# Performance work log

Measured on AMD Instinct MI355X. Metric: run time of the kernel, lower is better.

The kernel has to match this reference:

```python
import jax, jax.numpy as jnp
import numpy as np

HEADS = 8
DIM_HEAD = 64
SCALE = DIM_HEAD ** -0.5


def setup_inputs() -> dict:
    key = jax.random.key(0)
    ks = jax.random.split(key, 8)
    B, Nq, Nk, D = 4, 1024, 2048, 512
    inner = HEADS * DIM_HEAD  # 512
    x = jax.random.normal(ks[0], (B, Nq, D), dtype=jnp.float32)
    context = jax.random.normal(ks[1], (B, Nk, D), dtype=jnp.float32)
    bias = jax.random.normal(ks[2], (B, Nq, Nk), dtype=jnp.float32)
    s = D ** -0.5
    Wq = jax.random.normal(ks[3], (inner, D), dtype=jnp.float32) * s
    Wk = jax.random.normal(ks[4], (inner, D), dtype=jnp.float32) * s
    Wv = jax.random.normal(ks[5], (inner, D), dtype=jnp.float32) * s
    Wo = jax.random.normal(ks[6], (D, inner), dtype=jnp.float32) * s
    bo = jnp.zeros((D,), dtype=jnp.float32)
    return {"x": x, "context": context, "bias": bias,
            "Wq": Wq, "Wk": Wk, "Wv": Wv, "Wo": Wo, "bo": bo}


def reference(x, context, bias, Wq, Wk, Wv, Wo, bo):
    B, Nq, _ = x.shape
    # torch Linear: y = x @ W.T ; reshape (h d) -> b h n d
    q = (x @ Wq.T).reshape(B, Nq, HEADS, DIM_HEAD).transpose(0, 2, 1, 3)
    k = (context @ Wk.T).reshape(B, -1, HEADS, DIM_HEAD).transpose(0, 2, 1, 3)
    v = (context @ Wv.T).reshape(B, -1, HEADS, DIM_HEAD).transpose(0, 2, 1, 3)
    # explicit-score fallback path (bias supplied)
    scores = jnp.einsum('bhqd,bhkd->bhqk', q, k) * SCALE
    scores = scores + bias[:, None, :, :]  # 3D bias -> (B,1,Nq,Nk)
    attn = jax.nn.softmax(scores, axis=-1)
    out = jnp.einsum('bhqk,bhkd->bhqd', attn, v)
    out = out.transpose(0, 2, 1, 3).reshape(B, Nq, HEADS * DIM_HEAD)
    return out @ Wo.T + bo
```

## Files before the change

kernel.cpp:

```cpp
#include <hip/hip_runtime.h>

#define H 8
#define DH 64
#define NQ 1024
#define NK 2048
#define DIN 512
#define B 4
#define KSPLIT 2
#define KRANGE (NK / KSPLIT)
#define KTILES (KRANGE / 64)
#define BHNQ (B * H * NQ)

typedef __bf16 bf16;
typedef __bf16 bf16x8 __attribute__((ext_vector_type(8)));
typedef __bf16 bf16x4 __attribute__((ext_vector_type(4)));
typedef float floatx4 __attribute__((ext_vector_type(4)));

__device__ inline void gload16(const void* g, void* l) {
  __builtin_amdgcn_global_load_lds(
      (const __attribute__((address_space(1))) void*)g,
      (__attribute__((address_space(3))) void*)l, 16, 0, 0);
}

__global__ void cvt_all(const float* __restrict__ x, const float* __restrict__ ctx,
                        const float* __restrict__ wq, const float* __restrict__ wk,
                        const float* __restrict__ wv, const float* __restrict__ wo,
                        bf16* xb, bf16* cb, bf16* wqb, bf16* wkb, bf16* wvb, bf16* wob) {
  long i = ((long)blockIdx.x * 256 + threadIdx.x) * 4;
  const float* s; bf16* d; long o;
  if (i < 2097152)      { s = x;   d = xb;  o = i; }
  else if (i < 6291456) { s = ctx; d = cb;  o = i - 2097152; }
  else if (i < 6553600) { s = wq;  d = wqb; o = i - 6291456; }
  else if (i < 6815744) { s = wk;  d = wkb; o = i - 6553600; }
  else if (i < 7077888) { s = wv;  d = wvb; o = i - 6815744; }
  else                  { s = wo;  d = wob; o = i - 7077888; }
  float4 f = *(const float4*)(s + o);
  bf16x4 v = { (bf16)f.x, (bf16)f.y, (bf16)f.z, (bf16)f.w };
  *(bf16x4*)(d + o) = v;
}

__global__ __launch_bounds__(256) void gemm_qkv(
    const bf16* __restrict__ xb, const bf16* __restrict__ cb,
    const bf16* __restrict__ wqb, const bf16* __restrict__ wkb, const bf16* __restrict__ wvb,
    bf16* __restrict__ qb, bf16* __restrict__ kb, bf16* __restrict__ vtb) {
  const int which = blockIdx.z;
  if (which == 0 && blockIdx.y >= 32) return;
  const bf16* A = (which == 0) ? xb : cb;
  const bf16* W = (which == 0) ? wqb : ((which == 1) ? wkb : wvb);
  bf16* outb = (which == 0) ? qb : ((which == 1) ? kb : vtb);
  const int logT = (which == 0) ? 10 : 11;
  const float scale = (which == 0) ? 0.125f : 1.0f;
  const bool vmode = (which == 2);

  __shared__ bf16 Al[2][128 * 32];
  __shared__ bf16 Bl[2][128 * 32];
  const int t = threadIdx.x;
  const int lane = t & 63, w = t >> 6;
  const int ln = lane & 15, quad = lane >> 4;
  const int wm = (w >> 1) * 64, wn = (w & 1) * 64;
  const int rowBase = blockIdx.y * 128;
  const int colBase = blockIdx.x * 128;

  floatx4 acc[4][4] = {};
  const int c0 = t, c1 = t + 256;
  const int r0 = c0 >> 2, o0 = (c0 & 3) * 8;
  const int r1 = c1 >> 2, o1 = (c1 & 3) * 8;
  const bf16* Ab = A + (size_t)rowBase * DIN;
  const bf16* Wb = W + (size_t)colBase * DIN;

  gload16(Ab + (size_t)r0 * DIN + o0, &Al[0][c0 * 8]);
  gload16(Ab + (size_t)r1 * DIN + o1, &Al[0][c1 * 8]);
  gload16(Wb + (size_t)r0 * DIN + o0, &Bl[0][c0 * 8]);
  gload16(Wb + (size_t)r1 * DIN + o1, &Bl[0][c1 * 8]);
  __syncthreads();

  for (int k0 = 0; k0 < DIN; k0 += 32) {
    const int cur = (k0 >> 5) & 1, nxt = cur ^ 1;
    if (k0 + 32 < DIN) {
      gload16(Ab + (size_t)r0 * DIN + k0 + 32 + o0, &Al[nxt][c0 * 8]);
      gload16(Ab + (size_t)r1 * DIN + k0 + 32 + o1, &Al[nxt][c1 * 8]);
      gload16(Wb + (size_t)r0 * DIN + k0 + 32 + o0, &Bl[nxt][c0 * 8]);
      gload16(Wb + (size_t)r1 * DIN + k0 + 32 + o1, &Bl[nxt][c1 * 8]);
    }
    bf16x8 af[4], bfr[4];
#pragma unroll
    for (int i = 0; i < 4; i++)
      af[i] = *(const bf16x8*)&Al[cur][(wm + i * 16 + ln) * 32 + quad * 8];
#pragma unroll
    for (int j = 0; j < 4; j++)
      bfr[j] = *(const bf16x8*)&Bl[cur][(wn + j * 16 + ln) * 32 + quad * 8];
#pragma unroll
    for (int i = 0; i < 4; i++)
#pragma unroll
      for (int j = 0; j < 4; j++)
        acc[i][j] = __builtin_amdgcn_mfma_f32_16x16x32_bf16(af[i], bfr[j], acc[i][j], 0, 0, 0);
    __syncthreads();
  }

  const int T = 1 << logT;
#pragma unroll
  for (int i = 0; i < 4; i++)
#pragma unroll
    for (int j = 0; j < 4; j++)
#pragma unroll
      for (int r = 0; r < 4; r++) {
        const int m = rowBase + wm + i * 16 + quad * 4 + r;
        const int n = colBase + wn + j * 16 + ln;
        const float v = acc[i][j][r] * scale;
        const int bb = m >> logT, tok = m & (T - 1);
        const int hh = n >> 6, d = n & 63;
        if (!vmode)
          outb[((((size_t)(bb * H + hh)) << logT) + tok) * DH + d] = (bf16)v;
        else
          outb[(((size_t)(bb * H + hh) * DH + d) << logT) + tok] = (bf16)v;
      }
}

__global__ __launch_bounds__(128) void attn_fwd(
    const bf16* __restrict__ q, const bf16* __restrict__ k,
    const bf16* __restrict__ vt, const float* __restrict__ bias,
    float* __restrict__ op0, float* __restrict__ op1, float* __restrict__ lpart) {
  __shared__ bf16 KL[64 * 64];
  __shared__ bf16 VL[64 * 64];
  __shared__ bf16 Pl[2][16 * 64];
  const int tid = threadIdx.x;
  const int lane = tid & 63, w = tid >> 6;
  const int ln = lane & 15, quad = lane >> 4;
  const int hh = blockIdx.y;
  const int b = blockIdx.z >> 1, ks = blockIdx.z & 1;
  const int q0 = blockIdx.x * 32;
  const int k0 = ks * KRANGE;
  const size_t bh = (size_t)b * H + hh;
  const bf16* qp = q + bh * NQ * DH;
  const bf16* kp = k + bh * NK * DH;
  const bf16* vp = vt + bh * DH * NK;
  const float* bp = bias + ((size_t)b * NQ + q0 + w * 16 + quad * 4) * NK + ln;
  bf16* pl = &Pl[w][0];

  bf16x8 qf[2];
#pragma unroll
  for (int kc = 0; kc < 2; kc++)
    qf[kc] = *(const bf16x8*)(qp + (size_t)(q0 + w * 16 + ln) * DH + kc * 32 + quad * 8);

  floatx4 o[4] = {};
  floatx4 lac = {};
  const bf16x8 ones = {(bf16)1.f, (bf16)1.f, (bf16)1.f, (bf16)1.f,
                       (bf16)1.f, (bf16)1.f, (bf16)1.f, (bf16)1.f};
  constexpr float L2E = 1.44269504f;
  constexpr float OFF = 34.6246810f;

  for (int tt = 0; tt < KTILES; tt++) {
    const int nk0 = k0 + tt * 64;
#pragma unroll
    for (int s = 0; s < 4; s++) {
      const int i = s * 128 + tid;
      const int sr = i >> 3, sc = (i & 7) ^ (sr & 7);
      gload16(kp + (size_t)(nk0 + sr) * DH + sc * 8, &KL[i * 8]);
      gload16(vp + (size_t)sr * NK + nk0 + sc * 8, &VL[i * 8]);
    }
    float bc[4][4];
#pragma unroll
    for (int j = 0; j < 4; j++)
#pragma unroll
      for (int r = 0; r < 4; r++)
        bc[j][r] = bp[(size_t)r * NK + nk0 + j * 16];
    __syncthreads();

    floatx4 s4[4];
#pragma unroll
    for (int j = 0; j < 4; j++) {
      s4[j][0] = bc[j][0]; s4[j][1] = bc[j][1];
      s4[j][2] = bc[j][2]; s4[j][3] = bc[j][3];
    }
#pragma unroll
    for (int j = 0; j < 4; j++)
#pragma unroll
      for (int kc = 0; kc < 2; kc++) {
        const int kr = j * 16 + ln;
        bf16x8 kf = *(const bf16x8*)&KL[kr * 64 + (((kc * 4 + quad) ^ (kr & 7)) * 8)];
        s4[j] = __builtin_amdgcn_mfma_f32_16x16x32_bf16(qf[kc], kf, s4[j], 0, 0, 0);
      }

#pragma unroll
    for (int j = 0; j < 4; j++)
#pragma unroll
      for (int r = 0; r < 4; r++)
        s4[j][r] = exp2f(fmaf(s4[j][r], L2E, -OFF));

#pragma unroll
    for (int j = 0; j < 4; j++)
#pragma unroll
      for (int r = 0; r < 4; r++) {
        const int m = quad * 4 + r;
        pl[m * 64 + (((j * 2 + (ln >> 3)) ^ (m & 7)) * 8) + (ln & 7)] = (bf16)s4[j][r];
      }
    asm volatile("s_waitcnt lgkmcnt(0)" ::: "memory");
    bf16x8 pf[2];
#pragma unroll
    for (int kc = 0; kc < 2; kc++)
      pf[kc] = *(const bf16x8*)&pl[ln * 64 + (((kc * 4 + quad) ^ (ln & 7)) * 8)];

#pragma unroll
    for (int kc = 0; kc < 2; kc++)
      lac = __builtin_amdgcn_mfma_f32_16x16x32_bf16(pf[kc], ones, lac, 0, 0, 0);

#pragma unroll
    for (int jn = 0; jn < 4; jn++)
#pragma unroll
      for (int kc = 0; kc < 2; kc++) {
        const int vr = jn * 16 + ln;
        bf16x8 vf = *(const bf16x8*)&VL[vr * 64 + (((kc * 4 + quad) ^ (vr & 7)) * 8)];
        o[jn] = __builtin_amdgcn_mfma_f32_16x16x32_bf16(pf[kc], vf, o[jn], 0, 0, 0);
      }
    __syncthreads();
  }

  float* op = (ks ? op1 : op0) +
              ((size_t)b * NQ + q0 + w * 16 + quad * 4) * DIN + hh * 64 + ln;
#pragma unroll
  for (int jn = 0; jn < 4; jn++)
#pragma unroll
    for (int r = 0; r < 4; r++)
      op[(size_t)r * DIN + jn * 16] = o[jn][r];

  if (ln == 0) {
    float4 lv = {lac[0], lac[1], lac[2], lac[3]};
    *(float4*)&lpart[((size_t)ks * B * H + b * H + hh) * NQ + q0 + w * 16 + quad * 4] = lv;
  }
}

__global__ __launch_bounds__(256) void gemm_out(
    const float* __restrict__ op0, const float* __restrict__ op1,
    const float* __restrict__ lp, const bf16* __restrict__ W,
    float* __restrict__ outf, const float* __restrict__ bo) {
  __shared__ bf16 Al[2][128 * 32];
  __shared__ bf16 Bl[2][128 * 32];
  const int t = threadIdx.x;
  const int lane = t & 63, w = t >> 6;
  const int ln = lane & 15, quad = lane >> 4;
  const int wm = (w >> 1) * 64, wn = (w & 1) * 64;
  const int rowBase = blockIdx.y * 128;
  const int colBase = blockIdx.x * 128;

  floatx4 acc[4][4] = {};
  const int c0 = t, c1 = t + 256;
  const int r0 = c0 >> 2, o0 = (c0 & 3) * 8;
  const int r1 = c1 >> 2, o1 = (c1 & 3) * 8;
  const int m0 = rowBase + r0, m1 = rowBase + r1;
  const bf16* Wb = W + (size_t)colBase * DIN;

  float linv0[8], linv1[8];
#pragma unroll
  for (int h = 0; h < 8; h++) {
    const int i0 = ((m0 >> 10) * H + h) * NQ + (m0 & 1023);
    const int i1 = ((m1 >> 10) * H + h) * NQ + (m1 & 1023);
    linv0[h] = 1.0f / (lp[i0] + lp[BHNQ + i0]);
    linv1[h] = 1.0f / (lp[i1] + lp[BHNQ + i1]);
  }

#define STAGE_A(K0V, BUF)                                                      \
  {                                                                            \
    const float sA = linv0[(K0V) >> 6], sB = linv1[(K0V) >> 6];                \
    const float* pa0 = op0 + (size_t)m0 * DIN + (K0V) + o0;                    \
    const float* pa1 = op1 + (size_t)m0 * DIN + (K0V) + o0;                    \
    const float* pb0 = op0 + (size_t)m1 * DIN + (K0V) + o1;                    \
    const float* pb1 = op1 + (size_t)m1 * DIN + (K0V) + o1;                    \
    float4 xa = *(const float4*)pa0, xb2 = *(const float4*)(pa0 + 4);          \
    float4 ya = *(const float4*)pa1, yb = *(const float4*)(pa1 + 4);           \
    float4 za = *(const float4*)pb0, zb = *(const float4*)(pb0 + 4);           \
    float4 ua = *(const float4*)pb1, ub = *(const float4*)(pb1 + 4);           \
    bf16x8 v0 = {(bf16)((xa.x + ya.x) * sA), (bf16)((xa.y + ya.y) * sA),       \
                 (bf16)((xa.z + ya.z) * sA), (bf16)((xa.w + ya.w) * sA),       \
                 (bf16)((xb2.x + yb.x) * sA), (bf16)((xb2.y + yb.y) * sA),     \
                 (bf16)((xb2.z + yb.z) * sA), (bf16)((xb2.w + yb.w) * sA)};    \
    bf16x8 v1 = {(bf16)((za.x + ua.x) * sB), (bf16)((za.y + ua.y) * sB),       \
                 (bf16)((za.z + ua.z) * sB), (bf16)((za.w + ua.w) * sB),       \
                 (bf16)((zb.x + ub.x) * sB), (bf16)((zb.y + ub.y) * sB),       \
                 (bf16)((zb.z + ub.z) * sB), (bf16)((zb.w + ub.w) * sB)};      \
    *(bf16x8*)&Al[BUF][c0 * 8] = v0;                                           \
    *(bf16x8*)&Al[BUF][c1 * 8] = v1;                                           \
  }

  STAGE_A(0, 0);
  gload16(Wb + (size_t)r0 * DIN + o0, &Bl[0][c0 * 8]);
  gload16(Wb + (size_t)r1 * DIN + o1, &Bl[0][c1 * 8]);
  __syncthreads();

#pragma unroll
  for (int kk = 0; kk < 16; kk++) {
    const int cur = kk & 1, nxt = cur ^ 1;
    if (kk < 15) {
      const int k1 = (kk + 1) * 32;
      STAGE_A(k1, nxt);
      gload16(Wb + (size_t)r0 * DIN + k1 + o0, &Bl[nxt][c0 * 8]);
      gload16(Wb + (size_t)r1 * DIN + k1 + o1, &Bl[nxt][c1 * 8]);
    }
    bf16x8 af[4], bfr[4];
#pragma unroll
    for (int i = 0; i < 4; i++)
      af[i] = *(const bf16x8*)&Al[cur][(wm + i * 16 + ln) * 32 + quad * 8];
#pragma unroll
    for (int j = 0; j < 4; j++)
      bfr[j] = *(const bf16x8*)&Bl[cur][(wn + j * 16 + ln) * 32 + quad * 8];
#pragma unroll
    for (int i = 0; i < 4; i++)
#pragma unroll
      for (int j = 0; j < 4; j++)
        acc[i][j] = __builtin_amdgcn_mfma_f32_16x16x32_bf16(af[i], bfr[j], acc[i][j], 0, 0, 0);
    __syncthreads();
  }
#undef STAGE_A

#pragma unroll
  for (int i = 0; i < 4; i++)
#pragma unroll
    for (int j = 0; j < 4; j++)
#pragma unroll
      for (int r = 0; r < 4; r++) {
        const int m = rowBase + wm + i * 16 + quad * 4 + r;
        const int n = colBase + wn + j * 16 + ln;
        outf[(size_t)m * DIN + n] = acc[i][j][r] + bo[n];
      }
}

extern "C" void kernel_launch(void* const* d_in, const int* in_sizes, int n_in,
                              void* d_out, int out_size, void* d_ws, size_t ws_size,
                              hipStream_t stream) {
  const float* x    = (const float*)d_in[0];
  const float* ctx  = (const float*)d_in[1];
  const float* bias = (const float*)d_in[2];
  const float* Wq   = (const float*)d_in[3];
  const float* Wk   = (const float*)d_in[4];
  const float* Wv   = (const float*)d_in[5];
  const float* Wo   = (const float*)d_in[6];
  const float* bo   = (const float*)d_in[7];
  float* out = (float*)d_out;

  char* p = (char*)d_ws;
  bf16* xb   = (bf16*)(p + 0);
  bf16* cb   = (bf16*)(p + 4194304);
  bf16* wqb  = (bf16*)(p + 12582912);
  bf16* wkb  = (bf16*)(p + 13107200);
  bf16* wvb  = (bf16*)(p + 13631488);
  bf16* wob  = (bf16*)(p + 14155776);
  bf16* qb   = (bf16*)(p + 14680064);
  bf16* kb   = (bf16*)(p + 18874368);
  bf16* vtb  = (bf16*)(p + 27262976);
  float* op1 = (float*)(p + 35651584);
  float* lpart = (float*)(p + 44040192);
  float* op0 = (float*)cb;

  cvt_all<<<7168, 256, 0, stream>>>(x, ctx, Wq, Wk, Wv, Wo, xb, cb, wqb, wkb, wvb, wob);
  gemm_qkv<<<dim3(4, 64, 3), 256, 0, stream>>>(xb, cb, wqb, wkb, wvb, qb, kb, vtb);
  attn_fwd<<<dim3(NQ / 32, H, B * KSPLIT), 128, 0, stream>>>(qb, kb, vtb, bias, op0, op1, lpart);
  gemm_out<<<dim3(4, 32), 256, 0, stream>>>(op0, op1, lpart, wob, out, bo);
}
```

Measured before the change: 211.2 us.

## Retile GEMMs to 64-row blocks and double query rows per attention warp

The QKV and output projection GEMMs switch to 64x128 tiles, doubling the grid so more blocks fill the GPU. The V projection swaps MFMA operands so each lane writes consecutive tokens into the transposed V buffer, aiming for better store coalescing. The attention kernel has each warp handle 32 query rows instead of 16, reusing each K/V LDS fragment across two MFMAs, which halves K/V tile reloads and block count. The cost is more registers per attention thread, which may lower occupancy, and smaller GEMM tiles give less reuse per block.

Result: faster. 196.6 us (-6.9%).

```diff
diff --git a/kernel.cpp b/kernel.cpp
--- a/kernel.cpp
+++ b/kernel.cpp
@@ -44,7 +44,7 @@
     const bf16* __restrict__ wqb, const bf16* __restrict__ wkb, const bf16* __restrict__ wvb,
     bf16* __restrict__ qb, bf16* __restrict__ kb, bf16* __restrict__ vtb) {
   const int which = blockIdx.z;
-  if (which == 0 && blockIdx.y >= 32) return;
+  if (which == 0 && blockIdx.y >= 64) return;
   const bf16* A = (which == 0) ? xb : cb;
   const bf16* W = (which == 0) ? wqb : ((which == 1) ? wkb : wvb);
   bf16* outb = (which == 0) ? qb : ((which == 1) ? kb : vtb);
@@ -52,67 +52,79 @@
   const float scale = (which == 0) ? 0.125f : 1.0f;
   const bool vmode = (which == 2);
 
-  __shared__ bf16 Al[2][128 * 32];
+  __shared__ bf16 Al[2][64 * 32];
   __shared__ bf16 Bl[2][128 * 32];
   const int t = threadIdx.x;
   const int lane = t & 63, w = t >> 6;
   const int ln = lane & 15, quad = lane >> 4;
-  const int wm = (w >> 1) * 64, wn = (w & 1) * 64;
-  const int rowBase = blockIdx.y * 128;
+  const int wm = (w >> 1) * 32, wn = (w & 1) * 64;
+  const int rowBase = blockIdx.y * 64;
   const int colBase = blockIdx.x * 128;
 
-  floatx4 acc[4][4] = {};
+  floatx4 acc[2][4] = {};
+  const int rA = t >> 2, oA = (t & 3) * 8;
   const int c0 = t, c1 = t + 256;
-  const int r0 = c0 >> 2, o0 = (c0 & 3) * 8;
-  const int r1 = c1 >> 2, o1 = (c1 & 3) * 8;
+  const int rB0 = c0 >> 2, oB0 = (c0 & 3) * 8;
+  const int rB1 = c1 >> 2, oB1 = (c1 & 3) * 8;
   const bf16* Ab = A + (size_t)rowBase * DIN;
   const bf16* Wb = W + (size_t)colBase * DIN;
 
-  gload16(Ab + (size_t)r0 * DIN + o0, &Al[0][c0 * 8]);
-  gload16(Ab + (size_t)r1 * DIN + o1, &Al[0][c1 * 8]);
-  gload16(Wb + (size_t)r0 * DIN + o0, &Bl[0][c0 * 8]);
-  gload16(Wb + (size_t)r1 * DIN + o1, &Bl[0][c1 * 8]);
+  gload16(Ab + (size_t)rA * DIN + oA, &Al[0][t * 8]);
+  gload16(Wb + (size_t)rB0 * DIN + oB0, &Bl[0][c0 * 8]);
+  gload16(Wb + (size_t)rB1 * DIN + oB1, &Bl[0][c1 * 8]);
   __syncthreads();
 
   for (int k0 = 0; k0 < DIN; k0 += 32) {
     const int cur = (k0 >> 5) & 1, nxt = cur ^ 1;
     if (k0 + 32 < DIN) {
-      gload16(Ab + (size_t)r0 * DIN + k0 + 32 + o0, &Al[nxt][c0 * 8]);
-      gload16(Ab + (size_t)r1 * DIN + k0 + 32 + o1, &Al[nxt][c1 * 8]);
-      gload16(Wb + (size_t)r0 * DIN + k0 + 32 + o0, &Bl[nxt][c0 * 8]);
-      gload16(Wb + (size_t)r1 * DIN + k0 + 32 + o1, &Bl[nxt][c1 * 8]);
-    }
-    bf16x8 af[4], bfr[4];
-#pragma unroll
-    for (int i = 0; i < 4; i++)
+      gload16(Ab + (size_t)rA * DIN + k0 + 32 + oA, &Al[nxt][t * 8]);
+      gload16(Wb + (size_t)rB0 * DIN + k0 + 32 + oB0, &Bl[nxt][c0 * 8]);
+      gload16(Wb + (size_t)rB1 * DIN + k0 + 32 + oB1, &Bl[nxt][c1 * 8]);
+    }
+    bf16x8 af[2], bfr[4];
+#pragma unroll
+    for (int i = 0; i < 2; i++)
       af[i] = *(const bf16x8*)&Al[cur][(wm + i * 16 + ln) * 32 + quad * 8];
 #pragma unroll
     for (int j = 0; j < 4; j++)
       bfr[j] = *(const bf16x8*)&Bl[cur][(wn + j * 16 + ln) * 32 + quad * 8];
-#pragma unroll
-    for (int i = 0; i < 4; i++)
-#pragma unroll
-      for (int j = 0; j < 4; j++)
-        acc[i][j] = __builtin_amdgcn_mfma_f32_16x16x32_bf16(af[i], bfr[j], acc[i][j], 0, 0, 0);
+    if (!vmode) {
+#pragma unroll
+      for (int i = 0; i < 2; i++)
+#pragma unroll
+        for (int j = 0; j < 4; j++)
+          acc[i][j] = __builtin_amdgcn_mfma_f32_16x16x32_bf16(af[i], bfr[j], acc[i][j], 0, 0, 0);
+    } else {
+#pragma unroll
+      for (int i = 0; i < 2; i++)
+#pragma unroll
+        for (int j = 0; j < 4; j++)
+          acc[i][j] = __builtin_amdgcn_mfma_f32_16x16x32_bf16(bfr[j], af[i], acc[i][j], 0, 0, 0);
+    }
     __syncthreads();
   }
 
   const int T = 1 << logT;
 #pragma unroll
-  for (int i = 0; i < 4; i++)
+  for (int i = 0; i < 2; i++)
 #pragma unroll
     for (int j = 0; j < 4; j++)
 #pragma unroll
       for (int r = 0; r < 4; r++) {
-        const int m = rowBase + wm + i * 16 + quad * 4 + r;
-        const int n = colBase + wn + j * 16 + ln;
-        const float v = acc[i][j][r] * scale;
-        const int bb = m >> logT, tok = m & (T - 1);
-        const int hh = n >> 6, d = n & 63;
-        if (!vmode)
+        if (!vmode) {
+          const int m = rowBase + wm + i * 16 + quad * 4 + r;
+          const int n = colBase + wn + j * 16 + ln;
+          const float v = acc[i][j][r] * scale;
+          const int bb = m >> logT, tok = m & (T - 1);
+          const int hh = n >> 6, d = n & 63;
           outb[((((size_t)(bb * H + hh)) << logT) + tok) * DH + d] = (bf16)v;
-        else
-          outb[(((size_t)(bb * H + hh) * DH + d) << logT) + tok] = (bf16)v;
+        } else {
+          const int dg = colBase + wn + j * 16 + quad * 4 + r;
+          const int m = rowBase + wm + i * 16 + ln;
+          const int bb = m >> logT, tok = m & (T - 1);
+          const int hh = dg >> 6, d = dg & 63;
+          outb[(((size_t)(bb * H + hh) * DH + d) << logT) + tok] = (bf16)acc[i][j][r];
+        }
       }
 }
 
@@ -122,28 +134,29 @@
     float* __restrict__ op0, float* __restrict__ op1, float* __restrict__ lpart) {
   __shared__ bf16 KL[64 * 64];
   __shared__ bf16 VL[64 * 64];
-  __shared__ bf16 Pl[2][16 * 64];
+  __shared__ bf16 Pl[2][2][16 * 64];
   const int tid = threadIdx.x;
   const int lane = tid & 63, w = tid >> 6;
   const int ln = lane & 15, quad = lane >> 4;
   const int hh = blockIdx.y;
   const int b = blockIdx.z >> 1, ks = blockIdx.z & 1;
-  const int q0 = blockIdx.x * 32;
+  const int q0 = blockIdx.x * 64;
   const int k0 = ks * KRANGE;
   const size_t bh = (size_t)b * H + hh;
   const bf16* qp = q + bh * NQ * DH;
   const bf16* kp = k + bh * NK * DH;
   const bf16* vp = vt + bh * DH * NK;
-  const float* bp = bias + ((size_t)b * NQ + q0 + w * 16 + quad * 4) * NK + ln;
-  bf16* pl = &Pl[w][0];
-
-  bf16x8 qf[2];
-#pragma unroll
-  for (int kc = 0; kc < 2; kc++)
-    qf[kc] = *(const bf16x8*)(qp + (size_t)(q0 + w * 16 + ln) * DH + kc * 32 + quad * 8);
-
-  floatx4 o[4] = {};
-  floatx4 lac = {};
+  const float* bp = bias + ((size_t)b * NQ + q0 + w * 32 + quad * 4) * NK + ln;
+
+  bf16x8 qf[2][2];
+#pragma unroll
+  for (int s = 0; s < 2; s++)
+#pragma unroll
+    for (int kc = 0; kc < 2; kc++)
+      qf[s][kc] = *(const bf16x8*)(qp + (size_t)(q0 + w * 32 + s * 16 + ln) * DH + kc * 32 + quad * 8);
+
+  floatx4 o[2][4] = {};
+  floatx4 lac[2] = {};
   const bf16x8 ones = {(bf16)1.f, (bf16)1.f, (bf16)1.f, (bf16)1.f,
                        (bf16)1.f, (bf16)1.f, (bf16)1.f, (bf16)1.f};
   constexpr float L2E = 1.44269504f;
@@ -158,51 +171,64 @@
       gload16(kp + (size_t)(nk0 + sr) * DH + sc * 8, &KL[i * 8]);
       gload16(vp + (size_t)sr * NK + nk0 + sc * 8, &VL[i * 8]);
     }
-    float bc[4][4];
-#pragma unroll
-    for (int j = 0; j < 4; j++)
-#pragma unroll
-      for (int r = 0; r < 4; r++)
-        bc[j][r] = bp[(size_t)r * NK + nk0 + j * 16];
+    float bc[2][4][4];
+#pragma unroll
+    for (int s = 0; s < 2; s++)
+#pragma unroll
+      for (int j = 0; j < 4; j++)
+#pragma unroll
+        for (int r = 0; r < 4; r++)
+          bc[s][j][r] = bp[(size_t)(s * 16 + r) * NK + nk0 + j * 16];
     __syncthreads();
 
-    floatx4 s4[4];
-#pragma unroll
-    for (int j = 0; j < 4; j++) {
-      s4[j][0] = bc[j][0]; s4[j][1] = bc[j][1];
-      s4[j][2] = bc[j][2]; s4[j][3] = bc[j][3];
-    }
+    floatx4 s4[2][4];
+#pragma unroll
+    for (int s = 0; s < 2; s++)
+#pragma unroll
+      for (int j = 0; j < 4; j++) {
+        s4[s][j][0] = bc[s][j][0]; s4[s][j][1] = bc[s][j][1];
+        s4[s][j][2] = bc[s][j][2]; s4[s][j][3] = bc[s][j][3];
+      }
 #pragma unroll
     for (int j = 0; j < 4; j++)
 #pragma unroll
       for (int kc = 0; kc < 2; kc++) {
         const int kr = j * 16 + ln;
         bf16x8 kf = *(const bf16x8*)&KL[kr * 64 + (((kc * 4 + quad) ^ (kr & 7)) * 8)];
-        s4[j] = __builtin_amdgcn_mfma_f32_16x16x32_bf16(qf[kc], kf, s4[j], 0, 0, 0);
-      }
-
-#pragma unroll
-    for (int j = 0; j < 4; j++)
-#pragma unroll
-      for (int r = 0; r < 4; r++)
-        s4[j][r] = exp2f(fmaf(s4[j][r], L2E, -OFF));
-
-#pragma unroll
-    for (int j = 0; j < 4; j++)
-#pragma unroll
-      for (int r = 0; r < 4; r++) {
-        const int m = quad * 4 + r;
-        pl[m * 64 + (((j * 2 + (ln >> 3)) ^ (m & 7)) * 8) + (ln & 7)] = (bf16)s4[j][r];
-      }
+        s4[0][j] = __builtin_amdgcn_mfma_f32_16x16x32_bf16(qf[0][kc], kf, s4[0][j], 0, 0, 0);
+        s4[1][j] = __builtin_amdgcn_mfma_f32_16x16x32_bf16(qf[1][kc], kf, s4[1][j], 0, 0, 0);
+      }
+
+#pragma unroll
+    for (int s = 0; s < 2; s++)
+#pragma unroll
+      for (int j = 0; j < 4; j++)
+#pragma unroll
+        for (int r = 0; r < 4; r++)
+          s4[s][j][r] = exp2f(fmaf(s4[s][j][r], L2E, -OFF));
+
+#pragma unroll
+    for (int s = 0; s < 2; s++)
+#pragma unroll
+      for (int j = 0; j < 4; j++)
+#pragma unroll
+        for (int r = 0; r < 4; r++) {
+          const int m = quad * 4 + r;
+          Pl[w][s][m * 64 + (((j * 2 + (ln >> 3)) ^ (m & 7)) * 8) + (ln & 7)] = (bf16)s4[s][j][r];
+        }
     asm volatile("s_waitcnt lgkmcnt(0)" ::: "memory");
-    bf16x8 pf[2];
-#pragma unroll
-    for (int kc = 0; kc < 2; kc++)
-      pf[kc] = *(const bf16x8*)&pl[ln * 64 + (((kc * 4 + quad) ^ (ln & 7)) * 8)];
-
-#pragma unroll
-    for (int kc = 0; kc < 2; kc++)
-      lac = __builtin_amdgcn_mfma_f32_16x16x32_bf16(pf[kc], ones, lac, 0, 0, 0);
+    bf16x8 pf[2][2];
+#pragma unroll
+    for (int s = 0; s < 2; s++)
+#pragma unroll
+      for (int kc = 0; kc < 2; kc++)
+        pf[s][kc] = *(const bf16x8*)&Pl[w][s][ln * 64 + (((kc * 4 + quad) ^ (ln & 7)) * 8)];
+
+#pragma unroll
+    for (int s = 0; s < 2; s++)
+#pragma unroll
+      for (int kc = 0; kc < 2; kc++)
+        lac[s] = __builtin_amdgcn_mfma_f32_16x16x32_bf16(pf[s][kc], ones, lac[s], 0, 0, 0);
 
 #pragma unroll
     for (int jn = 0; jn < 4; jn++)
@@ -210,22 +236,25 @@
       for (int kc = 0; kc < 2; kc++) {
         const int vr = jn * 16 + ln;
         bf16x8 vf = *(const bf16x8*)&VL[vr * 64 + (((kc * 4 + quad) ^ (vr & 7)) * 8)];
-        o[jn] = __builtin_amdgcn_mfma_f32_16x16x32_bf16(pf[kc], vf, o[jn], 0, 0, 0);
+        o[0][jn] = __builtin_amdgcn_mfma_f32_16x16x32_bf16(pf[0][kc], vf, o[0][jn], 0, 0, 0);
+        o[1][jn] = __builtin_amdgcn_mfma_f32_16x16x32_bf16(pf[1][kc], vf, o[1][jn], 0, 0, 0);
       }
     __syncthreads();
   }
 
-  float* op = (ks ? op1 : op0) +
-              ((size_t)b * NQ + q0 + w * 16 + quad * 4) * DIN + hh * 64 + ln;
-#pragma unroll
-  for (int jn = 0; jn < 4; jn++)
-#pragma unroll
-    for (int r = 0; r < 4; r++)
-      op[(size_t)r * DIN + jn * 16] = o[jn][r];
-
-  if (ln == 0) {
-    float4 lv = {lac[0], lac[1], lac[2], lac[3]};
-    *(float4*)&lpart[((size_t)ks * B * H + b * H + hh) * NQ + q0 + w * 16 + quad * 4] = lv;
+#pragma unroll
+  for (int s = 0; s < 2; s++) {
+    float* op = (ks ? op1 : op0) +
+                ((size_t)b * NQ + q0 + w * 32 + s * 16 + quad * 4) * DIN + hh * 64 + ln;
+#pragma unroll
+    for (int jn = 0; jn < 4; jn++)
+#pragma unroll
+      for (int r = 0; r < 4; r++)
+        op[(size_t)r * DIN + jn * 16] = o[s][jn][r];
+    if (ln == 0) {
+      float4 lv = {lac[s][0], lac[s][1], lac[s][2], lac[s][3]};
+      *(float4*)&lpart[((size_t)ks * B * H + b * H + hh) * NQ + q0 + w * 32 + s * 16 + quad * 4] = lv;
+    }
   }
 }
 
@@ -233,57 +262,47 @@
     const float* __restrict__ op0, const float* __restrict__ op1,
     const float* __restrict__ lp, const bf16* __restrict__ W,
     float* __restrict__ outf, const float* __restrict__ bo) {
-  __shared__ bf16 Al[2][128 * 32];
+  __shared__ bf16 Al[2][64 * 32];
   __shared__ bf16 Bl[2][128 * 32];
   const int t = threadIdx.x;
   const int lane = t & 63, w = t >> 6;
   const int ln = lane & 15, quad = lane >> 4;
-  const int wm = (w >> 1) * 64, wn = (w & 1) * 64;
-  const int rowBase = blockIdx.y * 128;
+  const int wm = (w >> 1) * 32, wn = (w & 1) * 64;
+  const int rowBase = blockIdx.y * 64;
   const int colBase = blockIdx.x * 128;
 
-  floatx4 acc[4][4] = {};
+  floatx4 acc[2][4] = {};
+  const int rA = t >> 2, oA = (t & 3) * 8;
   const int c0 = t, c1 = t + 256;
-  const int r0 = c0 >> 2, o0 = (c0 & 3) * 8;
-  const int r1 = c1 >> 2, o1 = (c1 & 3) * 8;
-  const int m0 = rowBase + r0, m1 = rowBase + r1;
+  const int rB0 = c0 >> 2, oB0 = (c0 & 3) * 8;
+  const int rB1 = c1 >> 2, oB1 = (c1 & 3) * 8;
+  const int m0 = rowBase + rA;
   const bf16* Wb = W + (size_t)colBase * DIN;
 
-  float linv0[8], linv1[8];
+  float linv0[8];
 #pragma unroll
   for (int h = 0; h < 8; h++) {
     const int i0 = ((m0 >> 10) * H + h) * NQ + (m0 & 1023);
-    const int i1 = ((m1 >> 10) * H + h) * NQ + (m1 & 1023);
     linv0[h] = 1.0f / (lp[i0] + lp[BHNQ + i0]);
-    linv1[h] = 1.0f / (lp[i1] + lp[BHNQ + i1]);
   }
 
 #define STAGE_A(K0V, BUF)                                                      \
   {                                                                            \
-    const float sA = linv0[(K0V) >> 6], sB = linv1[(K0V) >> 6];                \
-    const float* pa0 = op0 + (size_t)m0 * DIN + (K0V) + o0;                    \
-    const float* pa1 = op1 + (size_t)m0 * DIN + (K0V) + o0;                    \
-    const float* pb0 = op0 + (size_t)m1 * DIN + (K0V) + o1;                    \
-    const float* pb1 = op1 + (size_t)m1 * DIN + (K0V) + o1;                    \
+    const float sA = linv0[(K0V) >> 6];                                        \
+    const float* pa0 = op0 + (size_t)m0 * DIN + (K0V) + oA;                    \
+    const float* pa1 = op1 + (size_t)m0 * DIN + (K0V) + oA;                    \
     float4 xa = *(const float4*)pa0, xb2 = *(const float4*)(pa0 + 4);          \
     float4 ya = *(const float4*)pa1, yb = *(const float4*)(pa1 + 4);           \
-    float4 za = *(const float4*)pb0, zb = *(const float4*)(pb0 + 4);           \
-    float4 ua = *(const float4*)pb1, ub = *(const float4*)(pb1 + 4);           \
     bf16x8 v0 = {(bf16)((xa.x + ya.x) * sA), (bf16)((xa.y + ya.y) * sA),       \
                  (bf16)((xa.z + ya.z) * sA), (bf16)((xa.w + ya.w) * sA),       \
                  (bf16)((xb2.x + yb.x) * sA), (bf16)((xb2.y + yb.y) * sA),     \
                  (bf16)((xb2.z + yb.z) * sA), (bf16)((xb2.w + yb.w) * sA)};    \
-    bf16x8 v1 = {(bf16)((za.x + ua.x) * sB), (bf16)((za.y + ua.y) * sB),       \
-                 (bf16)((za.z + ua.z) * sB), (bf16)((za.w + ua.w) * sB),       \
-                 (bf16)((zb.x + ub.x) * sB), (bf16)((zb.y + ub.y) * sB),       \
-                 (bf16)((zb.z + ub.z) * sB), (bf16)((zb.w + ub.w) * sB)};      \
-    *(bf16x8*)&Al[BUF][c0 * 8] = v0;                                           \
-    *(bf16x8*)&Al[BUF][c1 * 8] = v1;                                           \
+    *(bf16x8*)&Al[BUF][t * 8] = v0;                                            \
   }
 
   STAGE_A(0, 0);
-  gload16(Wb + (size_t)r0 * DIN + o0, &Bl[0][c0 * 8]);
-  gload16(Wb + (size_t)r1 * DIN + o1, &Bl[0][c1 * 8]);
+  gload16(Wb + (size_t)rB0 * DIN + oB0, &Bl[0][c0 * 8]);
+  gload16(Wb + (size_t)rB1 * DIN + oB1, &Bl[0][c1 * 8]);
   __syncthreads();
 
 #pragma unroll
@@ -292,18 +311,18 @@
     if (kk < 15) {
       const int k1 = (kk + 1) * 32;
       STAGE_A(k1, nxt);
-      gload16(Wb + (size_t)r0 * DIN + k1 + o0, &Bl[nxt][c0 * 8]);
-      gload16(Wb + (size_t)r1 * DIN + k1 + o1, &Bl[nxt][c1 * 8]);
-    }
-    bf16x8 af[4], bfr[4];
-#pragma unroll
-    for (int i = 0; i < 4; i++)
+      gload16(Wb + (size_t)rB0 * DIN + k1 + oB0, &Bl[nxt][c0 * 8]);
+      gload16(Wb + (size_t)rB1 * DIN + k1 + oB1, &Bl[nxt][c1 * 8]);
+    }
+    bf16x8 af[2], bfr[4];
+#pragma unroll
+    for (int i = 0; i < 2; i++)
       af[i] = *(const bf16x8*)&Al[cur][(wm + i * 16 + ln) * 32 + quad * 8];
 #pragma unroll
     for (int j = 0; j < 4; j++)
       bfr[j] = *(const bf16x8*)&Bl[cur][(wn + j * 16 + ln) * 32 + quad * 8];
 #pragma unroll
-    for (int i = 0; i < 4; i++)
+    for (int i = 0; i < 2; i++)
 #pragma unroll
       for (int j = 0; j < 4; j++)
         acc[i][j] = __builtin_amdgcn_mfma_f32_16x16x32_bf16(af[i], bfr[j], acc[i][j], 0, 0, 0);
@@ -312,7 +331,7 @@
 #undef STAGE_A
 
 #pragma unroll
-  for (int i = 0; i < 4; i++)
+  for (int i = 0; i < 2; i++)
 #pragma unroll
     for (int j = 0; j < 4; j++)
 #pragma unroll
@@ -351,7 +370,7 @@
   float* op0 = (float*)cb;
 
   cvt_all<<<7168, 256, 0, stream>>>(x, ctx, Wq, Wk, Wv, Wo, xb, cb, wqb, wkb, wvb, wob);
-  gemm_qkv<<<dim3(4, 64, 3), 256, 0, stream>>>(xb, cb, wqb, wkb, wvb, qb, kb, vtb);
-  attn_fwd<<<dim3(NQ / 32, H, B * KSPLIT), 128, 0, stream>>>(qb, kb, vtb, bias, op0, op1, lpart);
-  gemm_out<<<dim3(4, 32), 256, 0, stream>>>(op0, op1, lpart, wob, out, bo);
-}
+  gemm_qkv<<<dim3(4, 128, 3), 256, 0, stream>>>(xb, cb, wqb, wkb, wvb, qb, kb, vtb);
+  attn_fwd<<<dim3(NQ / 64, H, B * KSPLIT), 128, 0, stream>>>(qb, kb, vtb, bias, op0, op1, lpart);
+  gemm_out<<<dim3(4, 64), 256, 0, stream>>>(op0, op1, lpart, wob, out, bo);
+}
```
